# Optimization experiments

Hardware: AMD Instinct MI355X
Metric: run time of the kernel (lower is better)

Reference implementation:

```python
import jax, jax.numpy as jnp
import numpy as np

N_USERS, N_NEWS, N_ENT, N_REL, D, K, NNZ = 10000, 10000, 100000, 32, 64, 20, 500000

def setup_inputs() -> dict:
    key = jax.random.key(0)
    ks = jax.random.split(key, 10)
    return {
        "user_emb": jax.random.normal(ks[0], (N_USERS, D), jnp.float32),
        "news_embeding": jax.random.normal(ks[1], (N_NEWS, D), jnp.float32),
        "entity_emb": jax.random.normal(ks[2], (N_ENT, D), jnp.float32),
        "relation_emb": jax.random.normal(ks[3], (N_REL, D), jnp.float32),
        "news_entities": jax.random.randint(ks[4], (N_NEWS, K), 0, N_ENT),
        "news_relations": jnp.zeros((N_NEWS, K), jnp.int32),  # code forces relation id 0 for news
        "neigh_entities": jax.random.randint(ks[5], (N_ENT, K), 0, N_ENT),
        "neigh_relations": jax.random.randint(ks[6], (N_ENT, K), 0, N_REL),
        "interact_rows": jax.random.randint(ks[7], (NNZ,), 0, N_USERS),
        "interact_cols": jax.random.randint(ks[8], (NNZ,), 0, N_NEWS),
        "interact_vals": jax.random.uniform(ks[9], (NNZ,), jnp.float32),
    }

def _sim_hrt(head, tail, rel):
    # head: [N,D], tail/rel: [N,K,D]
    tail_rel = tail * rel                              # [N,K,D]
    head_rel = head[:, None, :] * rel                  # [N,K,D]
    # NOTE: original norms over the NEIGHBOR dim (dim=1), yielding [N,1,D]
    hnorm = jnp.sqrt(jnp.sum(head_rel * head_rel, axis=1))  # [N,D]
    att = jnp.einsum('nkd,nd->nk', tail_rel, hnorm)    # [N,K]
    return att * att

def _agg(head_emb, neigh_ent_emb, neigh_rel_emb):
    w = jax.nn.softmax(_sim_hrt(head_emb, neigh_ent_emb, neigh_rel_emb), axis=-1)
    return jnp.einsum('nk,nkd->nd', w, neigh_ent_emb)

def reference(user_emb, news_embeding, entity_emb, relation_emb,
              news_entities, news_relations, neigh_entities, neigh_relations,
              interact_rows, interact_cols, interact_vals):
    # news aggregation (newsid = arange -> identity gather on news_embeding)
    news_ne = entity_emb[news_entities]                # [N_news,K,D]
    news_nr = relation_emb[news_relations]             # [N_news,K,D]
    news_agg = _agg(news_embeding, news_ne, news_nr)   # [N_news,D]
    # entity aggregation (entities = arange -> identity gather on entity_emb)
    ent_ne = entity_emb[neigh_entities]                # [N_ent,K,D]
    ent_nr = relation_emb[neigh_relations]             # [N_ent,K,D]
    entity_agg = _agg(entity_emb, ent_ne, ent_nr)      # [N_ent,D]
    # user aggregation: sparse interact_mat @ news_agg via segment_sum
    gathered = interact_vals[:, None] * news_agg[interact_cols]  # [NNZ,D]
    user_agg = jax.ops.segment_sum(gathered, interact_rows, num_segments=N_USERS)
    score = jax.nn.softmax(user_emb @ news_agg.T, axis=-1)       # [N_users,N_news]
    user_agg = user_agg + (score @ news_agg) * user_agg
    return (news_agg, entity_agg, user_agg)
```

## Files before the change

kernel.cpp:

```cpp
#include <hip/hip_runtime.h>
#include <hip/hip_bf16.h>


#define DD 64
#define KK 20
#define NCHUNK 313
#define NSL 20
#define NSTRIP 157
#define NUPAD 10048
#define ATSTRIDE 10016
#define PST32 20

#define NUC 10000
#define NNC 10000
#define NEC 100000
#define NNZC 500000

#define K1_NEWS 1250
#define K1_CVTU 628
#define K1_HIST 512
#define K1_GRID (K1_NEWS + K1_CVTU + K1_HIST)
#define ATTN_BLOCKS 785
#define K3_FILL 512
#define K3_GRID (ATTN_BLOCKS + K3_FILL)
#define K4_GATHER 2500
#define K4_ENT 12500

typedef __attribute__((ext_vector_type(8))) short short8;
typedef __attribute__((ext_vector_type(4))) float f32x4;

__device__ __forceinline__ unsigned short f2bf(float x) {
    union { __hip_bfloat16 h; unsigned short u; } cv;
    cv.h = __float2bfloat16(x);
    return cv.u;
}
__device__ __forceinline__ float bfu2f(unsigned short u) {
    return __uint_as_float(((unsigned)u) << 16);
}
#define MFMA16(a, b, c) __builtin_amdgcn_mfma_f32_16x16x32_bf16((a), (b), (c), 0, 0, 0)

__device__ __forceinline__
void agg_body(const float* __restrict__ head_emb, const float* __restrict__ ent_emb,
              const float* __restrict__ rel_emb,
              const int* __restrict__ ent_idx, const int* __restrict__ rel_idx,
              float* __restrict__ outp, int bid)
{
    int w = threadIdx.x >> 6;
    int lane = threadIdx.x & 63;
    int half = lane >> 5;
    int l = lane & 31;
    int n0 = bid * 8 + w * 2;

    float2 head = *(const float2*)(head_emb + (long)(n0 + half) * DD + 2 * l);

    float2 tail[KK], trp[KK];
    float2 s2 = make_float2(0.f, 0.f);
#pragma unroll
    for (int k = 0; k < KK; ++k) {
        int ei0 = ent_idx[n0 * KK + k];
        int ei1 = ent_idx[(n0 + 1) * KK + k];
        int ri0 = rel_idx[n0 * KK + k];
        int ri1 = rel_idx[(n0 + 1) * KK + k];
        int e = half ? ei1 : ei0;
        int r = half ? ri1 : ri0;
        float2 rv = *(const float2*)(rel_emb + (long)r * DD + 2 * l);
        float2 tv = *(const float2*)(ent_emb + (long)e * DD + 2 * l);
        tail[k] = tv;
        trp[k] = make_float2(tv.x * rv.x, tv.y * rv.y);
        s2.x = fmaf(rv.x, rv.x, s2.x);
        s2.y = fmaf(rv.y, rv.y, s2.y);
    }
    float2 hn;
    hn.x = fabsf(head.x) * sqrtf(s2.x);
    hn.y = fabsf(head.y) * sqrtf(s2.y);

    float att[KK];
#pragma unroll
    for (int k = 0; k < KK; ++k) {
        float v = fmaf(trp[k].y, hn.y, trp[k].x * hn.x);
#pragma unroll
        for (int m = 1; m < 32; m <<= 1)
            v += __shfl_xor(v, m, 64);
        att[k] = v * v;
    }
    float mx = att[0];
#pragma unroll
    for (int k = 1; k < KK; ++k) mx = fmaxf(mx, att[k]);
    float den = 0.f;
#pragma unroll
    for (int k = 0; k < KK; ++k) { att[k] = __expf(att[k] - mx); den += att[k]; }
    float inv = 1.f / den;
    float2 o = make_float2(0.f, 0.f);
#pragma unroll
    for (int k = 0; k < KK; ++k) {
        o.x = fmaf(att[k], tail[k].x, o.x);
        o.y = fmaf(att[k], tail[k].y, o.y);
    }
    o.x *= inv; o.y *= inv;
    *(float2*)(outp + (long)(n0 + half) * DD + 2 * l) = o;
}

__global__ __launch_bounds__(256)
void k1_kernel(const float* __restrict__ news_emb, const float* __restrict__ ent_emb,
               const float* __restrict__ rel_emb,
               const int* __restrict__ news_entities, const int* __restrict__ news_relations,
               float* __restrict__ out_news,
               const float* __restrict__ user_emb, unsigned short* __restrict__ Ubf,
               const int* __restrict__ irows, int* __restrict__ cnt)
{
    int bid = blockIdx.x;
    if (bid < K1_NEWS) {
        agg_body(news_emb, ent_emb, rel_emb,
                 news_entities, news_relations, out_news, bid);
    } else if (bid < K1_NEWS + K1_CVTU) {
        int i = (bid - K1_NEWS) * 256 + threadIdx.x;
        int base = i * 4;
        float4 v = make_float4(0.f, 0.f, 0.f, 0.f);
        if (base + 3 < NUC * DD) v = *(const float4*)(user_emb + base);
        ushort4 o;
        o.x = f2bf(v.x); o.y = f2bf(v.y); o.z = f2bf(v.z); o.w = f2bf(v.w);
        *(ushort4*)(Ubf + base) = o;
    } else {
        int lb = bid - (K1_NEWS + K1_CVTU);
        for (int e = lb * 256 + threadIdx.x; e < NNZC; e += K1_HIST * 256)
            atomicAdd(&cnt[irows[e]], 1);
    }
}

__global__ __launch_bounds__(256)
void k2_kernel(const float* __restrict__ src, unsigned short* __restrict__ Bbf,
               unsigned short* __restrict__ AT,
               const int* __restrict__ cnt, int* __restrict__ offs, int* __restrict__ cur)
{
    __shared__ float T[128][65];
    __shared__ int ssum[256];
    int t = threadIdx.x;
    if (blockIdx.x < 79) {
        int nb = blockIdx.x * 128;
        const float4* s4 = (const float4*)src;
#pragma unroll
        for (int i = 0; i < 8; ++i) {
            int f = i * 256 + t;
            int row = f >> 4;
            int c4 = f & 15;
            int gr = nb + row;
            float4 v = make_float4(0.f, 0.f, 0.f, 0.f);
            if (gr < NNC) v = s4[(long)gr * 16 + c4];
            T[row][c4 * 4 + 0] = v.x;
            T[row][c4 * 4 + 1] = v.y;
            T[row][c4 * 4 + 2] = v.z;
            T[row][c4 * 4 + 3] = v.w;
        }
        __syncthreads();
#pragma unroll
        for (int i = 0; i < 8; ++i) {
            int f = i * 256 + t;
            int row = f >> 4;
            int q4 = f & 15;
            int gr = nb + row;
            if (gr < ATSTRIDE) {
                ushort4 ob;
                ob.x = f2bf(T[row][q4 * 4 + 0]);
                ob.y = f2bf(T[row][q4 * 4 + 1]);
                ob.z = f2bf(T[row][q4 * 4 + 2]);
                ob.w = f2bf(T[row][q4 * 4 + 3]);
                *(ushort4*)(Bbf + (long)gr * 64 + q4 * 4) = ob;
            }
        }
        int d = t >> 2;
        int seg = t & 3;
#pragma unroll
        for (int g = 0; g < 8; ++g) {
            int nl = seg * 32 + g * 4;
            int n = nb + nl;
            if (n + 3 < ATSTRIDE) {
                int base = seg * 32;
                ushort4 oh;
                oh.x = f2bf(T[base + 2 * g][d]);
                oh.y = f2bf(T[base + 16 + 2 * g][d]);
                oh.z = f2bf(T[base + 2 * g + 1][d]);
                oh.w = f2bf(T[base + 16 + 2 * g + 1][d]);
                *(ushort4*)(AT + (long)d * ATSTRIDE + n) = oh;
            }
        }
    } else {
        int loc[40];
        int s = 0;
#pragma unroll
        for (int i = 0; i < 40; ++i) { loc[i] = s; s += cnt[t * 40 + i]; }
        ssum[t] = s;
        __syncthreads();
        int val = s;
        for (int off = 1; off < 256; off <<= 1) {
            int v = (t >= off) ? ssum[t - off] : 0;
            __syncthreads();
            val += v;
            ssum[t] = val;
            __syncthreads();
        }
        int excl = val - s;
#pragma unroll
        for (int i = 0; i < 40; ++i) {
            int o = excl + loc[i];
            offs[t * 40 + i] = o;
            cur[t * 40 + i] = o;
        }
    }
}

__device__ __forceinline__
void attn_body(const unsigned short* __restrict__ Ubf,
               const unsigned short* __restrict__ Bbf,
               const unsigned short* __restrict__ ATbf,
               float* __restrict__ num, float* __restrict__ den,
               unsigned int* __restrict__ PuAll, int bid)
{
    int w = threadIdx.x >> 6;
    int lane = threadIdx.x & 63;
    int quad = lane >> 4;
    int l15 = lane & 15;
    int wid = bid * 4 + w;
    int strip = wid % NSTRIP;
    int slice = wid / NSTRIP;
    int user0 = strip * 64;

    short8 ua0[4], ua1[4];
#pragma unroll
    for (int t = 0; t < 4; ++t) {
        const short* up = (const short*)Ubf + ((long)(user0 + t * 16 + l15)) * 64;
        ua0[t] = *(const short8*)(up + quad * 8);
        ua1[t] = *(const short8*)(up + 32 + quad * 8);
    }

    f32x4 numC[4][4];
    float dena[4][4];
#pragma unroll
    for (int t = 0; t < 4; ++t)
#pragma unroll
        for (int c = 0; c < 4; ++c) {
            numC[t][c] = (f32x4){0.f, 0.f, 0.f, 0.f};
            dena[t][c] = 0.f;
        }

    for (int ch = slice; ch < NCHUNK; ch += NSL) {
        int nb = ch * 32;
        const short* bh = (const short*)Bbf + ((long)(nb + l15)) * 64;
        short8 b00 = *(const short8*)(bh + quad * 8);
        short8 b01 = *(const short8*)(bh + 32 + quad * 8);
        short8 b10 = *(const short8*)(bh + 16 * 64 + quad * 8);
        short8 b11 = *(const short8*)(bh + 16 * 64 + 32 + quad * 8);

        short8 vh[4];
#pragma unroll
        for (int c = 0; c < 4; ++c)
            vh[c] = *(const short8*)((const short*)ATbf +
                    ((long)(16 * c + l15)) * ATSTRIDE + nb + quad * 8);

        bool vlo = (nb + l15) < NNC;
        bool vhi = (nb + 16 + l15) < NNC;
        f32x4 z = {0.f, 0.f, 0.f, 0.f};
#pragma unroll
        for (int p = 0; p < 2; ++p) {
#pragma unroll
            for (int tt = 0; tt < 2; ++tt) {
                int t = p * 2 + tt;
                f32x4 Llo = MFMA16(ua0[t], b00, z);
                Llo = MFMA16(ua1[t], b01, Llo);
                f32x4 Lhi = MFMA16(ua0[t], b10, z);
                Lhi = MFMA16(ua1[t], b11, Lhi);
                unsigned int* Pt = PuAll + (w * 2 + tt) * (16 * PST32);
#pragma unroll
                for (int r = 0; r < 4; ++r) {
                    float plo = vlo ? __expf(fminf(Llo[r], 70.f)) : 0.f;
                    float phi = vhi ? __expf(fminf(Lhi[r], 70.f)) : 0.f;
                    __hip_bfloat162 pk2 = __float22bfloat162_rn(make_float2(plo, phi));
                    unsigned int pk;
                    __builtin_memcpy(&pk, &pk2, 4);
                    Pt[(quad * 4 + r) * PST32 + l15] = pk;
                    dena[t][r] += __uint_as_float(pk << 16)
                                + __uint_as_float(pk & 0xffff0000u);
                }
            }
            short8 ap[2];
#pragma unroll
            for (int tt = 0; tt < 2; ++tt)
                ap[tt] = *(const short8*)((const short*)(PuAll + (w * 2 + tt) * (16 * PST32)) +
                         l15 * (PST32 * 2) + quad * 8);
#pragma unroll
            for (int c = 0; c < 4; ++c)
#pragma unroll
                for (int tt = 0; tt < 2; ++tt)
                    numC[p * 2 + tt][c] = MFMA16(ap[tt], vh[c], numC[p * 2 + tt][c]);
        }
    }

#pragma unroll
    for (int t = 0; t < 4; ++t)
#pragma unroll
        for (int r = 0; r < 4; ++r) {
#pragma unroll
            for (int m = 1; m < 16; m <<= 1)
                dena[t][r] += __shfl_xor(dena[t][r], m, 64);
        }
    if (l15 == 0) {
#pragma unroll
        for (int t = 0; t < 4; ++t)
#pragma unroll
            for (int r = 0; r < 4; ++r)
                atomicAdd(&den[user0 + t * 16 + quad * 4 + r], dena[t][r]);
    }
#pragma unroll
    for (int t = 0; t < 4; ++t)
#pragma unroll
        for (int c = 0; c < 4; ++c)
#pragma unroll
            for (int r = 0; r < 4; ++r)
                atomicAdd(&num[(long)(user0 + t * 16 + quad * 4 + r) * DD + c * 16 + l15],
                          numC[t][c][r]);
}

__global__ __launch_bounds__(256)
void k3_kernel(const unsigned short* __restrict__ Ubf,
               const unsigned short* __restrict__ Bbf,
               const unsigned short* __restrict__ ATbf,
               float* __restrict__ num, float* __restrict__ den,
               const int* __restrict__ irows, int* __restrict__ cur,
               int* __restrict__ eid)
{
    __shared__ __align__(16) unsigned int Pu[8][16 * PST32];
    int bid = blockIdx.x;
    if (bid < ATTN_BLOCKS) {
        attn_body(Ubf, Bbf, ATbf, num, den, &Pu[0][0], bid);
    } else {
        int lb = bid - ATTN_BLOCKS;
        for (int e = lb * 256 + threadIdx.x; e < NNZC; e += K3_FILL * 256) {
            int p = atomicAdd(&cur[irows[e]], 1);
            eid[p] = e;
        }
    }
}

__global__ __launch_bounds__(256)
void k4_kernel(const int* __restrict__ offs, const int* __restrict__ eid,
               const int* __restrict__ cols, const float* __restrict__ vals,
               const float* __restrict__ A, float* __restrict__ seg,
               const float* __restrict__ ent_emb, const float* __restrict__ rel_emb,
               const int* __restrict__ neigh_entities, const int* __restrict__ neigh_relations,
               float* __restrict__ out_ent, int ent_blocks)
{
    int bid = blockIdx.x;
    if (bid < K4_GATHER) {
        int w = threadIdx.x >> 6;
        int lane = threadIdx.x & 63;
        int u = bid * 4 + w;
        if (u >= NUC) return;
        int s0 = offs[u], s1 = offs[u + 1];
        float acc = 0.f;
        for (int i = s0; i < s1; ++i) {
            int e = eid[i];
            float v = vals[e];
            int c = cols[e];
            acc = fmaf(v, A[(long)c * DD + lane], acc);
        }
        seg[(long)u * DD + lane] = acc;
    } else if (bid < K4_GATHER + ent_blocks) {
        int lb = bid - K4_GATHER;
        agg_body(ent_emb, ent_emb, rel_emb,
                 neigh_entities, neigh_relations, out_ent, lb);
    }
}

__global__ __launch_bounds__(256)
void agg_ent_kernel(const float* __restrict__ ent_emb, const float* __restrict__ rel_emb,
                    const int* __restrict__ ent_idx, const int* __restrict__ rel_idx,
                    float* __restrict__ outp)
{
    agg_body(ent_emb, ent_emb, rel_emb, ent_idx, rel_idx, outp, blockIdx.x);
}

__global__ __launch_bounds__(256)
void final_kernel(const float* __restrict__ seg, const float* __restrict__ num,
                  const float* __restrict__ den, float* __restrict__ out, int n_users)
{
    int t = blockIdx.x * 256 + threadIdx.x;
    if (t >= n_users * DD) return;
    int u = t >> 6;
    float s = seg[t];
    float o2 = num[t] / den[u];
    out[t] = fmaf(s, o2, s);
}

extern "C" void kernel_launch(void* const* d_in, const int* in_sizes, int n_in,
                              void* d_out, int out_size, void* d_ws, size_t ws_size,
                              hipStream_t stream)
{
    const float* user_emb = (const float*)d_in[0];
    const float* news_emb = (const float*)d_in[1];
    const float* ent_emb  = (const float*)d_in[2];
    const float* rel_emb  = (const float*)d_in[3];
    const int* news_entities   = (const int*)d_in[4];
    const int* news_relations  = (const int*)d_in[5];
    const int* neigh_entities  = (const int*)d_in[6];
    const int* neigh_relations = (const int*)d_in[7];
    const int* interact_rows   = (const int*)d_in[8];
    const int* interact_cols   = (const int*)d_in[9];
    const float* interact_vals = (const float*)d_in[10];

    const int NU = 10000, NN = 10000, NE = 100000;

    float* out_news = (float*)d_out;
    float* out_ent  = out_news + (long)NN * DD;
    float* out_user = out_ent + (long)NE * DD;

    const size_t BASIC_BYTES =
        (size_t)(640000 + 643072 + 10240 + 10240 + 10240 + 10240 + 500000) * 4 +
        (size_t)(643072 + 641024 + 641024) * 2;

    bool use_ws = (d_ws != nullptr) && (ws_size >= BASIC_BYTES);
    float* base = use_ws ? (float*)d_ws : out_ent;

    float* seg  = base;
    float* num  = seg + 640000;
    float* den  = num + 643072;
    int*   cnt  = (int*)(den + 10240);
    int*   offs = cnt + 10240;
    int*   cur  = offs + 10240;
    int*   eid  = cur + 10240;
    unsigned short* Ubf  = (unsigned short*)(eid + 500000);
    unsigned short* Bbf  = Ubf + 643072;
    unsigned short* ATbf = Bbf + 641024;

    hipMemsetAsync(num, 0, (size_t)(643072 + 10240 + 10240) * sizeof(float), stream);

    k1_kernel<<<K1_GRID, 256, 0, stream>>>(news_emb, ent_emb, rel_emb,
                                           news_entities, news_relations, out_news,
                                           user_emb, Ubf, interact_rows, cnt);
    k2_kernel<<<80, 256, 0, stream>>>(out_news, Bbf, ATbf, cnt, offs, cur);

    if (use_ws) {
        k3_kernel<<<K3_GRID, 256, 0, stream>>>(Ubf, Bbf, ATbf, num, den,
                                               interact_rows, cur, eid);
        k4_kernel<<<K4_GATHER + K4_ENT, 256, 0, stream>>>(
            offs, eid, interact_cols, interact_vals, out_news, seg,
            ent_emb, rel_emb, neigh_entities, neigh_relations, out_ent, K4_ENT);
        final_kernel<<<(NU * DD + 255) / 256, 256, 0, stream>>>(seg, num, den, out_user, NU);
    } else {
        k3_kernel<<<K3_GRID, 256, 0, stream>>>(Ubf, Bbf, ATbf, num, den,
                                               interact_rows, cur, eid);
        k4_kernel<<<K4_GATHER, 256, 0, stream>>>(
            offs, eid, interact_cols, interact_vals, out_news, seg,
            ent_emb, rel_emb, neigh_entities, neigh_relations, out_ent, 0);
        final_kernel<<<(NU * DD + 255) / 256, 256, 0, stream>>>(seg, num, den, out_user, NU);
        agg_ent_kernel<<<NE / 8, 256, 0, stream>>>(ent_emb, rel_emb,
                                                   neigh_entities, neigh_relations, out_ent);
    }
}
```

Baseline: 446.5 us.

## Fuse pipeline into cooperative persistent mega-kernel with grid syncs and work queue

Replaces the memset plus five kernel launches with a single cooperative persistent kernel of 768 blocks. Phases are separated by grid.sync(), and the final phase pulls attention, gather and entity-aggregation work from an atomic counter, so the stages share one dynamically balanced pool. The gather loop is also unrolled by four with independent accumulators. The aim is to remove launch gaps and tail idle time between stages. In exchange it adds grid-wide barrier costs and caps occupancy at 3 blocks per CU, and it falls back to the old multi-kernel path if the cooperative launch fails.

```diff
diff --git a/kernel.cpp b/kernel.cpp
--- a/kernel.cpp
+++ b/kernel.cpp
@@ -1,5 +1,8 @@
 #include <hip/hip_runtime.h>
 #include <hip/hip_bf16.h>
+#include <hip/hip_cooperative_groups.h>
+
+namespace cg = cooperative_groups;
 
 
 #define DD 64
@@ -7,7 +10,6 @@
 #define NCHUNK 313
 #define NSL 20
 #define NSTRIP 157
-#define NUPAD 10048
 #define ATSTRIDE 10016
 #define PST32 20
 
@@ -16,15 +18,18 @@
 #define NEC 100000
 #define NNZC 500000
 
-#define K1_NEWS 1250
-#define K1_CVTU 628
-#define K1_HIST 512
-#define K1_GRID (K1_NEWS + K1_CVTU + K1_HIST)
-#define ATTN_BLOCKS 785
-#define K3_FILL 512
-#define K3_GRID (ATTN_BLOCKS + K3_FILL)
-#define K4_GATHER 2500
-#define K4_ENT 12500
+#define GRID_MEGA 768
+#define A_NEWS 1250
+#define A_CVTU 628
+#define A_HIST 512
+#define A_TOTAL (A_NEWS + A_CVTU + A_HIST)
+#define B_TOTAL 80
+#define C_FILL 512
+#define D_ATTN 785
+#define D_GATHER 2500
+#define D_ENT 12500
+#define D_TOTAL (D_ATTN + D_GATHER + D_ENT)
+#define E_FINAL 625
 
 typedef __attribute__((ext_vector_type(8))) short short8;
 typedef __attribute__((ext_vector_type(4))) float f32x4;
@@ -100,112 +105,115 @@
     *(float2*)(outp + (long)(n0 + half) * DD + 2 * l) = o;
 }
 
-__global__ __launch_bounds__(256)
-void k1_kernel(const float* __restrict__ news_emb, const float* __restrict__ ent_emb,
-               const float* __restrict__ rel_emb,
-               const int* __restrict__ news_entities, const int* __restrict__ news_relations,
-               float* __restrict__ out_news,
-               const float* __restrict__ user_emb, unsigned short* __restrict__ Ubf,
-               const int* __restrict__ irows, int* __restrict__ cnt)
-{
-    int bid = blockIdx.x;
-    if (bid < K1_NEWS) {
-        agg_body(news_emb, ent_emb, rel_emb,
-                 news_entities, news_relations, out_news, bid);
-    } else if (bid < K1_NEWS + K1_CVTU) {
-        int i = (bid - K1_NEWS) * 256 + threadIdx.x;
-        int base = i * 4;
+__device__ __forceinline__
+void transpose_body(int vb, const float* __restrict__ src,
+                    unsigned short* __restrict__ Bbf, unsigned short* __restrict__ AT,
+                    float (*T)[65])
+{
+    int t = threadIdx.x;
+    int nb = vb * 128;
+    const float4* s4 = (const float4*)src;
+#pragma unroll
+    for (int i = 0; i < 8; ++i) {
+        int f = i * 256 + t;
+        int row = f >> 4;
+        int c4 = f & 15;
+        int gr = nb + row;
         float4 v = make_float4(0.f, 0.f, 0.f, 0.f);
-        if (base + 3 < NUC * DD) v = *(const float4*)(user_emb + base);
-        ushort4 o;
-        o.x = f2bf(v.x); o.y = f2bf(v.y); o.z = f2bf(v.z); o.w = f2bf(v.w);
-        *(ushort4*)(Ubf + base) = o;
-    } else {
-        int lb = bid - (K1_NEWS + K1_CVTU);
-        for (int e = lb * 256 + threadIdx.x; e < NNZC; e += K1_HIST * 256)
-            atomicAdd(&cnt[irows[e]], 1);
-    }
-}
-
-__global__ __launch_bounds__(256)
-void k2_kernel(const float* __restrict__ src, unsigned short* __restrict__ Bbf,
-               unsigned short* __restrict__ AT,
-               const int* __restrict__ cnt, int* __restrict__ offs, int* __restrict__ cur)
-{
-    __shared__ float T[128][65];
-    __shared__ int ssum[256];
+        if (gr < NNC) v = s4[(long)gr * 16 + c4];
+        T[row][c4 * 4 + 0] = v.x;
+        T[row][c4 * 4 + 1] = v.y;
+        T[row][c4 * 4 + 2] = v.z;
+        T[row][c4 * 4 + 3] = v.w;
+    }
+    __syncthreads();
+#pragma unroll
+    for (int i = 0; i < 8; ++i) {
+        int f = i * 256 + t;
+        int row = f >> 4;
+        int q4 = f & 15;
+        int gr = nb + row;
+        if (gr < ATSTRIDE) {
+            ushort4 ob;
+            ob.x = f2bf(T[row][q4 * 4 + 0]);
+            ob.y = f2bf(T[row][q4 * 4 + 1]);
+            ob.z = f2bf(T[row][q4 * 4 + 2]);
+            ob.w = f2bf(T[row][q4 * 4 + 3]);
+            *(ushort4*)(Bbf + (long)gr * 64 + q4 * 4) = ob;
+        }
+    }
+    int d = t >> 2;
+    int seg = t & 3;
+#pragma unroll
+    for (int g = 0; g < 8; ++g) {
+        int nl = seg * 32 + g * 4;
+        int n = nb + nl;
+        if (n + 3 < ATSTRIDE) {
+            int base = seg * 32;
+            ushort4 oh;
+            oh.x = f2bf(T[base + 2 * g][d]);
+            oh.y = f2bf(T[base + 16 + 2 * g][d]);
+            oh.z = f2bf(T[base + 2 * g + 1][d]);
+            oh.w = f2bf(T[base + 16 + 2 * g + 1][d]);
+            *(ushort4*)(AT + (long)d * ATSTRIDE + n) = oh;
+        }
+    }
+    __syncthreads();
+}
+
+__device__ __forceinline__
+void scan_body(const int* __restrict__ cnt, int* __restrict__ offs,
+               int* __restrict__ cur, int* __restrict__ ssum)
+{
     int t = threadIdx.x;
-    if (blockIdx.x < 79) {
-        int nb = blockIdx.x * 128;
-        const float4* s4 = (const float4*)src;
-#pragma unroll
-        for (int i = 0; i < 8; ++i) {
-            int f = i * 256 + t;
-            int row = f >> 4;
-            int c4 = f & 15;
-            int gr = nb + row;
-            float4 v = make_float4(0.f, 0.f, 0.f, 0.f);
-            if (gr < NNC) v = s4[(long)gr * 16 + c4];
-            T[row][c4 * 4 + 0] = v.x;
-            T[row][c4 * 4 + 1] = v.y;
-            T[row][c4 * 4 + 2] = v.z;
-            T[row][c4 * 4 + 3] = v.w;
-        }
+    int loc[40];
+    int s = 0;
+#pragma unroll
+    for (int i = 0; i < 40; ++i) { loc[i] = s; s += cnt[t * 40 + i]; }
+    ssum[t] = s;
+    __syncthreads();
+    int val = s;
+    for (int off = 1; off < 256; off <<= 1) {
+        int v = (t >= off) ? ssum[t - off] : 0;
         __syncthreads();
-#pragma unroll
-        for (int i = 0; i < 8; ++i) {
-            int f = i * 256 + t;
-            int row = f >> 4;
-            int q4 = f & 15;
-            int gr = nb + row;
-            if (gr < ATSTRIDE) {
-                ushort4 ob;
-                ob.x = f2bf(T[row][q4 * 4 + 0]);
-                ob.y = f2bf(T[row][q4 * 4 + 1]);
-                ob.z = f2bf(T[row][q4 * 4 + 2]);
-                ob.w = f2bf(T[row][q4 * 4 + 3]);
-                *(ushort4*)(Bbf + (long)gr * 64 + q4 * 4) = ob;
-            }
-        }
-        int d = t >> 2;
-        int seg = t & 3;
-#pragma unroll
-        for (int g = 0; g < 8; ++g) {
-            int nl = seg * 32 + g * 4;
-            int n = nb + nl;
-            if (n + 3 < ATSTRIDE) {
-                int base = seg * 32;
-                ushort4 oh;
-                oh.x = f2bf(T[base + 2 * g][d]);
-                oh.y = f2bf(T[base + 16 + 2 * g][d]);
-                oh.z = f2bf(T[base + 2 * g + 1][d]);
-                oh.w = f2bf(T[base + 16 + 2 * g + 1][d]);
-                *(ushort4*)(AT + (long)d * ATSTRIDE + n) = oh;
-            }
-        }
-    } else {
-        int loc[40];
-        int s = 0;
-#pragma unroll
-        for (int i = 0; i < 40; ++i) { loc[i] = s; s += cnt[t * 40 + i]; }
-        ssum[t] = s;
+        val += v;
+        ssum[t] = val;
         __syncthreads();
-        int val = s;
-        for (int off = 1; off < 256; off <<= 1) {
-            int v = (t >= off) ? ssum[t - off] : 0;
-            __syncthreads();
-            val += v;
-            ssum[t] = val;
-            __syncthreads();
-        }
-        int excl = val - s;
-#pragma unroll
-        for (int i = 0; i < 40; ++i) {
-            int o = excl + loc[i];
-            offs[t * 40 + i] = o;
-            cur[t * 40 + i] = o;
-        }
-    }
+    }
+    int excl = val - s;
+#pragma unroll
+    for (int i = 0; i < 40; ++i) {
+        int o = excl + loc[i];
+        offs[t * 40 + i] = o;
+        cur[t * 40 + i] = o;
+    }
+}
+
+__device__ __forceinline__
+void gather_body(int vb, const int* __restrict__ offs, const int* __restrict__ eid,
+                 const int* __restrict__ cols, const float* __restrict__ vals,
+                 const float* __restrict__ A, float* __restrict__ seg)
+{
+    int w = threadIdx.x >> 6;
+    int lane = threadIdx.x & 63;
+    int u = vb * 4 + w;
+    int s0 = offs[u], s1 = offs[u + 1];
+    float a0 = 0.f, a1 = 0.f, a2 = 0.f, a3 = 0.f;
+    int i = s0;
+    for (; i + 3 < s1; i += 4) {
+        int e0 = eid[i], e1 = eid[i + 1], e2 = eid[i + 2], e3 = eid[i + 3];
+        float v0 = vals[e0], v1 = vals[e1], v2 = vals[e2], v3 = vals[e3];
+        int c0 = cols[e0], c1 = cols[e1], c2 = cols[e2], c3 = cols[e3];
+        a0 = fmaf(v0, A[(long)c0 * DD + lane], a0);
+        a1 = fmaf(v1, A[(long)c1 * DD + lane], a1);
+        a2 = fmaf(v2, A[(long)c2 * DD + lane], a2);
+        a3 = fmaf(v3, A[(long)c3 * DD + lane], a3);
+    }
+    for (; i < s1; ++i) {
+        int e = eid[i];
+        a0 = fmaf(vals[e], A[(long)cols[e] * DD + lane], a0);
+    }
+    seg[(long)u * DD + lane] = (a0 + a1) + (a2 + a3);
 }
 
 __device__ __forceinline__
@@ -319,6 +327,147 @@
                           numC[t][c][r]);
 }
 
+__global__ __launch_bounds__(256, 3)
+void mega_kernel(const float* __restrict__ user_emb, const float* __restrict__ news_emb,
+                 const float* __restrict__ ent_emb, const float* __restrict__ rel_emb,
+                 const int* __restrict__ news_entities, const int* __restrict__ news_relations,
+                 const int* __restrict__ neigh_entities, const int* __restrict__ neigh_relations,
+                 const int* __restrict__ interact_rows, const int* __restrict__ interact_cols,
+                 const float* __restrict__ interact_vals,
+                 float* __restrict__ out_news, float* __restrict__ out_ent,
+                 float* __restrict__ out_user, float* __restrict__ base)
+{
+    float* seg  = base;
+    float* num  = seg + 640000;
+    float* den  = num + 643072;
+    int*   cnt  = (int*)(den + 10240);
+    int*   offs = cnt + 10240;
+    int*   cur  = offs + 10240;
+    int*   eid  = cur + 10240;
+    unsigned short* Ubf  = (unsigned short*)(eid + 500000);
+    unsigned short* Bbf  = Ubf + 643072;
+    unsigned short* ATbf = Bbf + 641024;
+    int* wctr = (int*)(ATbf + 641024);
+
+    __shared__ __align__(16) char smem[33280];
+    __shared__ int s_vb;
+
+    cg::grid_group grid = cg::this_grid();
+    int bid = blockIdx.x;
+    int tid = threadIdx.x;
+
+    for (int i = bid * 256 + tid; i < 643072 + 10240 + 10240; i += GRID_MEGA * 256)
+        num[i] = 0.f;
+    if (bid == 0 && tid == 0) atomicExch(wctr, 0);
+    grid.sync();
+
+    for (int vb = bid; vb < A_TOTAL; vb += GRID_MEGA) {
+        if (vb < A_NEWS) {
+            agg_body(news_emb, ent_emb, rel_emb,
+                     news_entities, news_relations, out_news, vb);
+        } else if (vb < A_NEWS + A_CVTU) {
+            int i = (vb - A_NEWS) * 256 + tid;
+            int bse = i * 4;
+            float4 v = make_float4(0.f, 0.f, 0.f, 0.f);
+            if (bse + 3 < NUC * DD) v = *(const float4*)(user_emb + bse);
+            ushort4 o;
+            o.x = f2bf(v.x); o.y = f2bf(v.y); o.z = f2bf(v.z); o.w = f2bf(v.w);
+            *(ushort4*)(Ubf + bse) = o;
+        } else {
+            int lb = vb - (A_NEWS + A_CVTU);
+            for (int e = lb * 256 + tid; e < NNZC; e += A_HIST * 256)
+                atomicAdd(&cnt[interact_rows[e]], 1);
+        }
+    }
+    grid.sync();
+
+    for (int vb = bid; vb < B_TOTAL; vb += GRID_MEGA) {
+        if (vb < 79)
+            transpose_body(vb, out_news, Bbf, ATbf, (float(*)[65])smem);
+        else
+            scan_body(cnt, offs, cur, (int*)smem);
+    }
+    grid.sync();
+
+    for (int vb = bid; vb < C_FILL; vb += GRID_MEGA) {
+        for (int e = vb * 256 + tid; e < NNZC; e += C_FILL * 256) {
+            int p = atomicAdd(&cur[interact_rows[e]], 1);
+            eid[p] = e;
+        }
+    }
+    grid.sync();
+
+    for (;;) {
+        if (tid == 0) s_vb = atomicAdd(wctr, 1);
+        __syncthreads();
+        int vb = s_vb;
+        __syncthreads();
+        if (vb >= D_TOTAL) break;
+        if (vb < D_ATTN) {
+            attn_body(Ubf, Bbf, ATbf, num, den, (unsigned int*)smem, vb);
+        } else if (vb < D_ATTN + D_GATHER) {
+            gather_body(vb - D_ATTN, offs, eid, interact_cols, interact_vals,
+                        out_news, seg);
+        } else {
+            agg_body(ent_emb, ent_emb, rel_emb, neigh_entities, neigh_relations,
+                     out_ent, vb - (D_ATTN + D_GATHER));
+        }
+    }
+    grid.sync();
+
+    for (int vb = bid; vb < E_FINAL; vb += GRID_MEGA) {
+        int bse = (vb * 256 + tid) * 4;
+        int u = bse >> 6;
+        float dv = den[u];
+        float4 s = *(const float4*)(seg + bse);
+        float4 n = *(const float4*)(num + bse);
+        float4 o;
+        o.x = fmaf(s.x, n.x / dv, s.x);
+        o.y = fmaf(s.y, n.y / dv, s.y);
+        o.z = fmaf(s.z, n.z / dv, s.z);
+        o.w = fmaf(s.w, n.w / dv, s.w);
+        *(float4*)(out_user + bse) = o;
+    }
+}
+
+__global__ __launch_bounds__(256)
+void k1_kernel(const float* __restrict__ news_emb, const float* __restrict__ ent_emb,
+               const float* __restrict__ rel_emb,
+               const int* __restrict__ news_entities, const int* __restrict__ news_relations,
+               float* __restrict__ out_news,
+               const float* __restrict__ user_emb, unsigned short* __restrict__ Ubf,
+               const int* __restrict__ irows, int* __restrict__ cnt)
+{
+    int bid = blockIdx.x;
+    if (bid < A_NEWS) {
+        agg_body(news_emb, ent_emb, rel_emb, news_entities, news_relations, out_news, bid);
+    } else if (bid < A_NEWS + A_CVTU) {
+        int i = (bid - A_NEWS) * 256 + threadIdx.x;
+        int bse = i * 4;
+        float4 v = make_float4(0.f, 0.f, 0.f, 0.f);
+        if (bse + 3 < NUC * DD) v = *(const float4*)(user_emb + bse);
+        ushort4 o;
+        o.x = f2bf(v.x); o.y = f2bf(v.y); o.z = f2bf(v.z); o.w = f2bf(v.w);
+        *(ushort4*)(Ubf + bse) = o;
+    } else {
+        int lb = bid - (A_NEWS + A_CVTU);
+        for (int e = lb * 256 + threadIdx.x; e < NNZC; e += A_HIST * 256)
+            atomicAdd(&cnt[irows[e]], 1);
+    }
+}
+
+__global__ __launch_bounds__(256)
+void k2_kernel(const float* __restrict__ src, unsigned short* __restrict__ Bbf,
+               unsigned short* __restrict__ AT,
+               const int* __restrict__ cnt, int* __restrict__ offs, int* __restrict__ cur)
+{
+    __shared__ __align__(16) char smem[33280];
+    if (blockIdx.x < 79)
+        transpose_body(blockIdx.x, src, Bbf, AT, (float(*)[65])smem);
+    else
+        scan_body(cnt, offs, cur, (int*)smem);
+}
+
 __global__ __launch_bounds__(256)
 void k3_kernel(const unsigned short* __restrict__ Ubf,
                const unsigned short* __restrict__ Bbf,
@@ -329,11 +478,11 @@
 {
     __shared__ __align__(16) unsigned int Pu[8][16 * PST32];
     int bid = blockIdx.x;
-    if (bid < ATTN_BLOCKS) {
+    if (bid < D_ATTN) {
         attn_body(Ubf, Bbf, ATbf, num, den, &Pu[0][0], bid);
     } else {
-        int lb = bid - ATTN_BLOCKS;
-        for (int e = lb * 256 + threadIdx.x; e < NNZC; e += K3_FILL * 256) {
+        int lb = bid - D_ATTN;
+        for (int e = lb * 256 + threadIdx.x; e < NNZC; e += C_FILL * 256) {
             int p = atomicAdd(&cur[irows[e]], 1);
             eid[p] = e;
         }
@@ -349,24 +498,11 @@
                float* __restrict__ out_ent, int ent_blocks)
 {
     int bid = blockIdx.x;
-    if (bid < K4_GATHER) {
-        int w = threadIdx.x >> 6;
-        int lane = threadIdx.x & 63;
-        int u = bid * 4 + w;
-        if (u >= NUC) return;
-        int s0 = offs[u], s1 = offs[u + 1];
-        float acc = 0.f;
-        for (int i = s0; i < s1; ++i) {
-            int e = eid[i];
-            float v = vals[e];
-            int c = cols[e];
-            acc = fmaf(v, A[(long)c * DD + lane], acc);
-        }
-        seg[(long)u * DD + lane] = acc;
-    } else if (bid < K4_GATHER + ent_blocks) {
-        int lb = bid - K4_GATHER;
-        agg_body(ent_emb, ent_emb, rel_emb,
-                 neigh_entities, neigh_relations, out_ent, lb);
+    if (bid < D_GATHER) {
+        gather_body(bid, offs, eid, cols, vals, A, seg);
+    } else if (bid < D_GATHER + ent_blocks) {
+        agg_body(ent_emb, ent_emb, rel_emb, neigh_entities, neigh_relations,
+                 out_ent, bid - D_GATHER);
     }
 }
 
@@ -414,7 +550,7 @@
 
     const size_t BASIC_BYTES =
         (size_t)(640000 + 643072 + 10240 + 10240 + 10240 + 10240 + 500000) * 4 +
-        (size_t)(643072 + 641024 + 641024) * 2;
+        (size_t)(643072 + 641024 + 641024) * 2 + 64;
 
     bool use_ws = (d_ws != nullptr) && (ws_size >= BASIC_BYTES);
     float* base = use_ws ? (float*)d_ws : out_ent;
@@ -430,24 +566,34 @@
     unsigned short* Bbf  = Ubf + 643072;
     unsigned short* ATbf = Bbf + 641024;
 
+    if (use_ws) {
+        void* kargs[] = {
+            (void*)&user_emb, (void*)&news_emb, (void*)&ent_emb, (void*)&rel_emb,
+            (void*)&news_entities, (void*)&news_relations,
+            (void*)&neigh_entities, (void*)&neigh_relations,
+            (void*)&interact_rows, (void*)&interact_cols, (void*)&interact_vals,
+            (void*)&out_news, (void*)&out_ent, (void*)&out_user, (void*)&base
+        };
+        hipError_t err = hipLaunchCooperativeKernel(
+            reinterpret_cast<const void*>(mega_kernel),
+            dim3(GRID_MEGA), dim3(256), kargs, 0, stream);
+        if (err == hipSuccess) return;
+    }
+
     hipMemsetAsync(num, 0, (size_t)(643072 + 10240 + 10240) * sizeof(float), stream);
-
-    k1_kernel<<<K1_GRID, 256, 0, stream>>>(news_emb, ent_emb, rel_emb,
+    k1_kernel<<<A_TOTAL, 256, 0, stream>>>(news_emb, ent_emb, rel_emb,
                                            news_entities, news_relations, out_news,
                                            user_emb, Ubf, interact_rows, cnt);
-    k2_kernel<<<80, 256, 0, stream>>>(out_news, Bbf, ATbf, cnt, offs, cur);
-
+    k2_kernel<<<B_TOTAL, 256, 0, stream>>>(out_news, Bbf, ATbf, cnt, offs, cur);
+    k3_kernel<<<D_ATTN + C_FILL, 256, 0, stream>>>(Ubf, Bbf, ATbf, num, den,
+                                                   interact_rows, cur, eid);
     if (use_ws) {
-        k3_kernel<<<K3_GRID, 256, 0, stream>>>(Ubf, Bbf, ATbf, num, den,
-                                               interact_rows, cur, eid);
-        k4_kernel<<<K4_GATHER + K4_ENT, 256, 0, stream>>>(
+        k4_kernel<<<D_GATHER + D_ENT, 256, 0, stream>>>(
             offs, eid, interact_cols, interact_vals, out_news, seg,
-            ent_emb, rel_emb, neigh_entities, neigh_relations, out_ent, K4_ENT);
+            ent_emb, rel_emb, neigh_entities, neigh_relations, out_ent, D_ENT);
         final_kernel<<<(NU * DD + 255) / 256, 256, 0, stream>>>(seg, num, den, out_user, NU);
     } else {
-        k3_kernel<<<K3_GRID, 256, 0, stream>>>(Ubf, Bbf, ATbf, num, den,
-                                               interact_rows, cur, eid);
-        k4_kernel<<<K4_GATHER, 256, 0, stream>>>(
+        k4_kernel<<<D_GATHER, 256, 0, stream>>>(
             offs, eid, interact_cols, interact_vals, out_news, seg,
             ent_emb, rel_emb, neigh_entities, neigh_relations, out_ent, 0);
         final_kernel<<<(NU * DD + 255) / 256, 256, 0, stream>>>(seg, num, den, out_user, NU);
```

After: 908.2 us. 103% more time.

## Split user gather into own kernel, fuse final with entity agg, double work per block

Applied to the files above, without the earlier changes.

The user-side segment gather moves into its own kernel and is unrolled four ways with separate accumulators, which adds memory-level parallelism. The final combine is vectorized to float4 and co-scheduled with entity aggregation in a new fused kernel, so the separate final_kernel launch is dropped. Each aggregation block now processes two 8-row groups, halving grid sizes for the news and entity aggregations. This changes which work overlaps: entity aggregation now waits for the gather instead of running alongside it. Larger per-block work may also reduce occupancy-driven latency hiding.

```diff
diff --git a/kernel.cpp b/kernel.cpp
--- a/kernel.cpp
+++ b/kernel.cpp
@@ -7,7 +7,6 @@
 #define NCHUNK 313
 #define NSL 20
 #define NSTRIP 157
-#define NUPAD 10048
 #define ATSTRIDE 10016
 #define PST32 20
 
@@ -16,7 +15,7 @@
 #define NEC 100000
 #define NNZC 500000
 
-#define K1_NEWS 1250
+#define K1_NEWS 625
 #define K1_CVTU 628
 #define K1_HIST 512
 #define K1_GRID (K1_NEWS + K1_CVTU + K1_HIST)
@@ -24,7 +23,9 @@
 #define K3_FILL 512
 #define K3_GRID (ATTN_BLOCKS + K3_FILL)
 #define K4_GATHER 2500
-#define K4_ENT 12500
+#define K5_FINAL 625
+#define K5_ENT 6250
+#define K5_GRID (K5_FINAL + K5_ENT)
 
 typedef __attribute__((ext_vector_type(8))) short short8;
 typedef __attribute__((ext_vector_type(4))) float f32x4;
@@ -110,16 +111,18 @@
 {
     int bid = blockIdx.x;
     if (bid < K1_NEWS) {
-        agg_body(news_emb, ent_emb, rel_emb,
-                 news_entities, news_relations, out_news, bid);
+        agg_body(news_emb, ent_emb, rel_emb, news_entities, news_relations,
+                 out_news, 2 * bid);
+        agg_body(news_emb, ent_emb, rel_emb, news_entities, news_relations,
+                 out_news, 2 * bid + 1);
     } else if (bid < K1_NEWS + K1_CVTU) {
         int i = (bid - K1_NEWS) * 256 + threadIdx.x;
-        int base = i * 4;
+        int bse = i * 4;
         float4 v = make_float4(0.f, 0.f, 0.f, 0.f);
-        if (base + 3 < NUC * DD) v = *(const float4*)(user_emb + base);
+        if (bse + 3 < NUC * DD) v = *(const float4*)(user_emb + bse);
         ushort4 o;
         o.x = f2bf(v.x); o.y = f2bf(v.y); o.z = f2bf(v.z); o.w = f2bf(v.w);
-        *(ushort4*)(Ubf + base) = o;
+        *(ushort4*)(Ubf + bse) = o;
     } else {
         int lb = bid - (K1_NEWS + K1_CVTU);
         for (int e = lb * 256 + threadIdx.x; e < NNZC; e += K1_HIST * 256)
@@ -341,32 +344,58 @@
 }
 
 __global__ __launch_bounds__(256)
-void k4_kernel(const int* __restrict__ offs, const int* __restrict__ eid,
-               const int* __restrict__ cols, const float* __restrict__ vals,
-               const float* __restrict__ A, float* __restrict__ seg,
+void gather_kernel(const int* __restrict__ offs, const int* __restrict__ eid,
+                   const int* __restrict__ cols, const float* __restrict__ vals,
+                   const float* __restrict__ A, float* __restrict__ seg)
+{
+    int w = threadIdx.x >> 6;
+    int lane = threadIdx.x & 63;
+    int u = blockIdx.x * 4 + w;
+    int s0 = offs[u], s1 = offs[u + 1];
+    float a0 = 0.f, a1 = 0.f, a2 = 0.f, a3 = 0.f;
+    int i = s0;
+    for (; i + 3 < s1; i += 4) {
+        int e0 = eid[i], e1 = eid[i + 1], e2 = eid[i + 2], e3 = eid[i + 3];
+        float v0 = vals[e0], v1 = vals[e1], v2 = vals[e2], v3 = vals[e3];
+        int c0 = cols[e0], c1 = cols[e1], c2 = cols[e2], c3 = cols[e3];
+        a0 = fmaf(v0, A[(long)c0 * DD + lane], a0);
+        a1 = fmaf(v1, A[(long)c1 * DD + lane], a1);
+        a2 = fmaf(v2, A[(long)c2 * DD + lane], a2);
+        a3 = fmaf(v3, A[(long)c3 * DD + lane], a3);
+    }
+    for (; i < s1; ++i) {
+        int e = eid[i];
+        a0 = fmaf(vals[e], A[(long)cols[e] * DD + lane], a0);
+    }
+    seg[(long)u * DD + lane] = (a0 + a1) + (a2 + a3);
+}
+
+__global__ __launch_bounds__(256)
+void k5_kernel(const float* __restrict__ seg, const float* __restrict__ num,
+               const float* __restrict__ den, float* __restrict__ out_user,
                const float* __restrict__ ent_emb, const float* __restrict__ rel_emb,
                const int* __restrict__ neigh_entities, const int* __restrict__ neigh_relations,
                float* __restrict__ out_ent, int ent_blocks)
 {
     int bid = blockIdx.x;
-    if (bid < K4_GATHER) {
-        int w = threadIdx.x >> 6;
-        int lane = threadIdx.x & 63;
-        int u = bid * 4 + w;
-        if (u >= NUC) return;
-        int s0 = offs[u], s1 = offs[u + 1];
-        float acc = 0.f;
-        for (int i = s0; i < s1; ++i) {
-            int e = eid[i];
-            float v = vals[e];
-            int c = cols[e];
-            acc = fmaf(v, A[(long)c * DD + lane], acc);
-        }
-        seg[(long)u * DD + lane] = acc;
-    } else if (bid < K4_GATHER + ent_blocks) {
-        int lb = bid - K4_GATHER;
-        agg_body(ent_emb, ent_emb, rel_emb,
-                 neigh_entities, neigh_relations, out_ent, lb);
+    if (bid < K5_FINAL) {
+        int bse = (bid * 256 + threadIdx.x) * 4;
+        int u = bse >> 6;
+        float dv = den[u];
+        float4 s = *(const float4*)(seg + bse);
+        float4 n = *(const float4*)(num + bse);
+        float4 o;
+        o.x = fmaf(s.x, n.x / dv, s.x);
+        o.y = fmaf(s.y, n.y / dv, s.y);
+        o.z = fmaf(s.z, n.z / dv, s.z);
+        o.w = fmaf(s.w, n.w / dv, s.w);
+        *(float4*)(out_user + bse) = o;
+    } else if (bid < K5_FINAL + ent_blocks) {
+        int lb = bid - K5_FINAL;
+        agg_body(ent_emb, ent_emb, rel_emb, neigh_entities, neigh_relations,
+                 out_ent, 2 * lb);
+        agg_body(ent_emb, ent_emb, rel_emb, neigh_entities, neigh_relations,
+                 out_ent, 2 * lb + 1);
     }
 }
 
@@ -375,7 +404,8 @@
                     const int* __restrict__ ent_idx, const int* __restrict__ rel_idx,
                     float* __restrict__ outp)
 {
-    agg_body(ent_emb, ent_emb, rel_emb, ent_idx, rel_idx, outp, blockIdx.x);
+    agg_body(ent_emb, ent_emb, rel_emb, ent_idx, rel_idx, outp, 2 * blockIdx.x);
+    agg_body(ent_emb, ent_emb, rel_emb, ent_idx, rel_idx, outp, 2 * blockIdx.x + 1);
 }
 
 __global__ __launch_bounds__(256)
@@ -436,22 +466,18 @@
                                            news_entities, news_relations, out_news,
                                            user_emb, Ubf, interact_rows, cnt);
     k2_kernel<<<80, 256, 0, stream>>>(out_news, Bbf, ATbf, cnt, offs, cur);
-
+    k3_kernel<<<K3_GRID, 256, 0, stream>>>(Ubf, Bbf, ATbf, num, den,
+                                           interact_rows, cur, eid);
+    gather_kernel<<<K4_GATHER, 256, 0, stream>>>(offs, eid, interact_cols,
+                                                 interact_vals, out_news, seg);
     if (use_ws) {
-        k3_kernel<<<K3_GRID, 256, 0, stream>>>(Ubf, Bbf, ATbf, num, den,
-                                               interact_rows, cur, eid);
-        k4_kernel<<<K4_GATHER + K4_ENT, 256, 0, stream>>>(
-            offs, eid, interact_cols, interact_vals, out_news, seg,
-            ent_emb, rel_emb, neigh_entities, neigh_relations, out_ent, K4_ENT);
+        k5_kernel<<<K5_GRID, 256, 0, stream>>>(seg, num, den, out_user,
+                                               ent_emb, rel_emb,
+                                               neigh_entities, neigh_relations,
+                                               out_ent, K5_ENT);
+    } else {
         final_kernel<<<(NU * DD + 255) / 256, 256, 0, stream>>>(seg, num, den, out_user, NU);
-    } else {
-        k3_kernel<<<K3_GRID, 256, 0, stream>>>(Ubf, Bbf, ATbf, num, den,
-                                               interact_rows, cur, eid);
-        k4_kernel<<<K4_GATHER, 256, 0, stream>>>(
-            offs, eid, interact_cols, interact_vals, out_news, seg,
-            ent_emb, rel_emb, neigh_entities, neigh_relations, out_ent, 0);
-        final_kernel<<<(NU * DD + 255) / 256, 256, 0, stream>>>(seg, num, den, out_user, NU);
-        agg_ent_kernel<<<NE / 8, 256, 0, stream>>>(ent_emb, rel_emb,
-                                                   neigh_entities, neigh_relations, out_ent);
-    }
-}
+        agg_ent_kernel<<<NE / 16, 256, 0, stream>>>(ent_emb, rel_emb,
+                                                    neigh_entities, neigh_relations, out_ent);
+    }
+}
```

Measured after the change: 456.0 us. 2.1% more time.
